# Kernel tuning notes

Measured on AMD Instinct MI355X. Metric: run time of the kernel, lower is better.

## Reference

```python
import jax, jax.numpy as jnp
import numpy as np

H = 32        # num_attention_heads
KVH = 8       # num_key_value_heads
D = 64        # head_dim
HID = 2048    # hidden_size
G = H // KVH  # num_key_value_groups


def setup_inputs() -> dict:
    key = jax.random.key(0)
    k1, k2, k3, k4, k5 = jax.random.split(key, 5)
    B, S = 1, 2048
    s = 1.0 / np.sqrt(HID)
    return {
        "hidden_states": jax.random.normal(k1, (B, S, HID), dtype=jnp.float32),
        "attention_mask": jnp.ones((B, S), dtype=jnp.int32),
        "Wq": jax.random.normal(k2, (H * D, HID), dtype=jnp.float32) * s,
        "Wk": jax.random.normal(k3, (KVH * D, HID), dtype=jnp.float32) * s,
        "Wv": jax.random.normal(k4, (KVH * D, HID), dtype=jnp.float32) * s,
        "Wo": jax.random.normal(k5, (HID, HID), dtype=jnp.float32) * s,
    }


def reference(hidden_states, attention_mask, Wq, Wk, Wv, Wo):
    B, S, _ = hidden_states.shape
    dtype = hidden_states.dtype

    q = (hidden_states @ Wq.T).reshape(B, S, H, D).transpose(0, 2, 1, 3)     # [B,H,S,D]
    k = (hidden_states @ Wk.T).reshape(B, S, KVH, D).transpose(0, 2, 1, 3)   # [B,KVH,S,D]
    v = (hidden_states @ Wv.T).reshape(B, S, KVH, D).transpose(0, 2, 1, 3)

    # repeat_interleave over head dim: each KV head serves G query heads
    k = jnp.repeat(k, G, axis=1)  # [B,H,S,D]
    v = jnp.repeat(v, G, axis=1)

    scores = jnp.einsum('bhqd,bhkd->bhqk', q, k) / np.sqrt(D)  # [B,H,S,S]

    causal = jnp.tril(jnp.ones((S, S), dtype=dtype))                # [S,S]
    am = attention_mask.astype(dtype)[:, None, None, :]              # [B,1,1,S]
    mask = am * causal[None, None, :, :]                             # [B,1,S,S]
    mask = (1.0 - mask) * jnp.finfo(dtype).min
    scores = scores + mask                                           # broadcast over heads

    weights = jax.nn.softmax(scores, axis=-1)
    attn = jnp.einsum('bhqk,bhkd->bhqd', weights, v)                 # [B,H,S,D]
    attn = attn.transpose(0, 2, 1, 3).reshape(B, S, HID)
    return attn @ Wo.T
```

## Files before the change

kernel.cpp:

```cpp
#include <hip/hip_runtime.h>
#include <hip/hip_bf16.h>
#include <math.h>

typedef __attribute__((ext_vector_type(4))) float f32x4;
typedef __attribute__((ext_vector_type(16))) float f32x16;
typedef __attribute__((ext_vector_type(8))) short bf16x8;
typedef __attribute__((ext_vector_type(4))) short s16x4;
typedef __attribute__((ext_vector_type(4))) unsigned int u32x4;
typedef __attribute__((ext_vector_type(2))) unsigned int u32x2;
typedef short s16;
typedef unsigned int u32;
typedef unsigned short u16;

#define S_LEN 2048
#define HIDN  2048
#define QKVW  3072
#define NH    32
#define NKVH  8
#define HD    64

__device__ __forceinline__ s16 f2bf(float f) {
  unsigned int u = __float_as_uint(f);
  unsigned int lsb = (u >> 16) & 1u;
  u += 0x7fffu + lsb;
  return (s16)(u >> 16);
}

__device__ __forceinline__ u32 cvtpk(float lo, float hi) {
  u32 r;
  asm("v_cvt_pk_bf16_f32 %0, %1, %2" : "=v"(r) : "v"(lo), "v"(hi));
  return r;
}

__device__ __forceinline__ void gload16(const void* g, void* l) {
  __builtin_amdgcn_global_load_lds(
      (const __attribute__((address_space(1))) void*)g,
      (__attribute__((address_space(3))) void*)l, 16, 0, 0);
}

__device__ __forceinline__ void pls(u32& a, u32& b) {
  asm volatile("v_permlane32_swap_b32 %0, %1" : "+v"(a), "+v"(b));
}

__device__ __forceinline__ int swz7(int row) { return (row ^ (row >> 3)) & 7; }

__global__ __launch_bounds__(256) void cvt_all(const float* __restrict__ h,
                                               const float* __restrict__ wq,
                                               const float* __restrict__ wk,
                                               const float* __restrict__ wv,
                                               const float* __restrict__ wo,
                                               s16x4* __restrict__ dst) {
  int i = blockIdx.x * 256 + threadIdx.x;
  const float* src; int off;
  if (i < 1048576)      { src = h;  off = i; }
  else if (i < 2097152) { src = wq; off = i - 1048576; }
  else if (i < 2359296) { src = wk; off = i - 2097152; }
  else if (i < 2621440) { src = wv; off = i - 2359296; }
  else                  { src = wo; off = i - 2621440; }
  if (i < 3670016) {
    float4 f = reinterpret_cast<const float4*>(src)[off];
    s16x4 o;
    o.x = f2bf(f.x); o.y = f2bf(f.y); o.z = f2bf(f.z); o.w = f2bf(f.w);
    dst[i] = o;
  }
}

__device__ __forceinline__ void storeC(s16* C, size_t idx, float v)   { C[idx] = f2bf(v); }
__device__ __forceinline__ void storeC(float* C, size_t idx, float v) { C[idx] = v; }

template <typename OUT_T>
__global__ __launch_bounds__(512) void gemm_bt(const s16* __restrict__ A,
                                               const s16* __restrict__ B,
                                               OUT_T* __restrict__ C,
                                               int M, int N, int K, int gridX) {
  __shared__ alignas(16) s16 As[2][8192];
  __shared__ alignas(16) s16 Bs[2][8192];

  const int nwg  = (M >> 7) * gridX;
  const int flat = blockIdx.x;
  const int q8   = nwg >> 3;
  const int swz  = (flat & 7) * q8 + (flat >> 3);
  const int bm   = (swz / gridX) * 128;
  const int bn   = (swz % gridX) * 128;

  const int t    = threadIdx.x;
  const int lane = t & 63;
  const int w    = t >> 6;
  const int wr   = (w >> 2) * 64;
  const int wc   = (w & 3) * 32;
  const int lr   = lane & 15;
  const int lg   = lane >> 4;

  const int srow0 = (w * 2) * 8 + (lane >> 3);
  const int srow1 = (w * 2 + 1) * 8 + (lane >> 3);
  const int sl0   = ((lane & 7) ^ swz7(srow0)) * 8;
  const int sl1   = ((lane & 7) ^ swz7(srow1)) * 8;

  f32x4 acc[4][2];
#pragma unroll
  for (int m = 0; m < 4; ++m)
#pragma unroll
    for (int n = 0; n < 2; ++n)
      acc[m][n] = (f32x4){0.f, 0.f, 0.f, 0.f};

  const int nK = K >> 6;
  int buf = 0;

  {
    gload16(&A[(size_t)(bm + srow0) * K + sl0], (char*)As[0] + (w * 2) * 1024);
    gload16(&A[(size_t)(bm + srow1) * K + sl1], (char*)As[0] + (w * 2 + 1) * 1024);
    gload16(&B[(size_t)(bn + srow0) * K + sl0], (char*)Bs[0] + (w * 2) * 1024);
    gload16(&B[(size_t)(bn + srow1) * K + sl1], (char*)Bs[0] + (w * 2 + 1) * 1024);
  }
  __syncthreads();

  for (int ki = 0; ki < nK; ++ki) {
    if (ki + 1 < nK) {
      const int kt = (ki + 1) << 6;
      gload16(&A[(size_t)(bm + srow0) * K + kt + sl0], (char*)As[buf ^ 1] + (w * 2) * 1024);
      gload16(&A[(size_t)(bm + srow1) * K + kt + sl1], (char*)As[buf ^ 1] + (w * 2 + 1) * 1024);
      gload16(&B[(size_t)(bn + srow0) * K + kt + sl0], (char*)Bs[buf ^ 1] + (w * 2) * 1024);
      gload16(&B[(size_t)(bn + srow1) * K + kt + sl1], (char*)Bs[buf ^ 1] + (w * 2 + 1) * 1024);
    }

    bf16x8 af[4][2], bfr[2][2];
#pragma unroll
    for (int kk = 0; kk < 2; ++kk) {
#pragma unroll
      for (int m = 0; m < 4; ++m) {
        int row = wr + m * 16 + lr;
        af[m][kk] = *(bf16x8*)((char*)As[buf] + row * 128 + (((kk * 4 + lg) ^ swz7(row)) << 4));
      }
#pragma unroll
      for (int n = 0; n < 2; ++n) {
        int row = wc + n * 16 + lr;
        bfr[n][kk] = *(bf16x8*)((char*)Bs[buf] + row * 128 + (((kk * 4 + lg) ^ swz7(row)) << 4));
      }
    }

    __builtin_amdgcn_s_setprio(1);
#pragma unroll
    for (int m = 0; m < 4; ++m)
#pragma unroll
      for (int n = 0; n < 2; ++n)
#pragma unroll
        for (int kk = 0; kk < 2; ++kk)
          acc[m][n] = __builtin_amdgcn_mfma_f32_16x16x32_bf16(af[m][kk], bfr[n][kk], acc[m][n], 0, 0, 0);
    __builtin_amdgcn_s_setprio(0);

    __syncthreads();
    buf ^= 1;
  }

#pragma unroll
  for (int m = 0; m < 4; ++m)
#pragma unroll
    for (int n = 0; n < 2; ++n) {
      int row = bm + wr + m * 16 + lg * 4;
      int col = bn + wc + n * 16 + lr;
#pragma unroll
      for (int j = 0; j < 4; ++j)
        storeC(C, (size_t)(row + j) * N + col, acc[m][n][j]);
    }
}

__global__ __launch_bounds__(512) void attn_kernel(
    const s16* __restrict__ QKV,
    const int* __restrict__ am,
    s16* __restrict__ Ob) {
  __shared__ alignas(16) char smem[65536];
  __shared__ float2 mlb[4][64];

  const int t    = threadIdx.x;
  const int g    = t >> 8;
  const int tg   = t & 255;
  const int lane = t & 63;
  const int w    = tg >> 6;
  const int col  = lane & 31;
  const int hi   = lane >> 5;

  const int hk = blockIdx.x;
  const int p  = blockIdx.y;
  const int h  = hk * 4 + w;
  const int kbase = 2048 + hk * 64;
  const int vbase = 2560 + hk * 64;
  const float CF = 0.18033688f;

  const int krow   = lane >> 3;
  const int kslotb = lane & 7;
  const int vkv    = 2 * (tg >> 3);
  const int vd8    = (tg & 7) * 8;

  for (int phase = 0; phase < 2; ++phase) {
    const int qt = phase ? p : 63 - p;
    const int nt = (qt >> 1) + 1;
    const int R  = (nt + 1) >> 1;
    const int qrow = qt * 32 + col;

    bf16x8 qf[4];
#pragma unroll
    for (int ds = 0; ds < 4; ++ds)
      qf[ds] = *(const bf16x8*)&QKV[(size_t)qrow * QKVW + h * 64 + ds * 16 + hi * 8];

    if (g < nt) {
      char* Kn = smem + (g * 2 + 0) * 16384;
      char* Vn = Kn + 8192;
#pragma unroll
      for (int pp = 0; pp < 2; ++pp) {
        int c   = w * 2 + pp;
        int row = c * 8 + krow;
        int slot = kslotb ^ swz7(row);
        gload16(&QKV[(size_t)(g * 64 + row) * QKVW + kbase + slot * 8], Kn + c * 1024);
      }
      bf16x8 va = *(const bf16x8*)&QKV[(size_t)(g * 64 + vkv) * QKVW + vbase + vd8];
      bf16x8 vb = *(const bf16x8*)&QKV[(size_t)(g * 64 + vkv + 1) * QKVW + vbase + vd8];
#pragma unroll
      for (int i = 0; i < 8; ++i) {
        int d = vd8 + i;
        u32 pk = (u32)(u16)va[i] | ((u32)(u16)vb[i] << 16);
        *(u32*)&Vn[(d * 128 + vkv * 2) ^ (swz7(d) << 4)] = pk;
      }
    }
    int acur = am[g * 64 + lane];

    float m_i = -1e30f, l_part = 0.f;
    f32x16 Oacc[2];
#pragma unroll
    for (int b = 0; b < 2; ++b)
#pragma unroll
      for (int i = 0; i < 16; ++i) Oacc[b][i] = 0.f;
    __syncthreads();

    for (int it = 0; it < R; ++it) {
      const int buf  = it & 1;
      const int tile = 2 * it + g;
      const bool valid = (tile < nt);
      const int kv0  = tile * 64;
      const bool pre = (tile + 2 < nt);

      char* Kc = smem + (g * 2 + buf) * 16384;
      char* Vc = Kc + 8192;
      char* Kn = smem + (g * 2 + (buf ^ 1)) * 16384;
      char* Vn = Kn + 8192;

      bf16x8 va, vb;
      int anext = 0;
      if (pre) {
        const int nk0 = kv0 + 128;
#pragma unroll
        for (int pp = 0; pp < 2; ++pp) {
          int c   = w * 2 + pp;
          int row = c * 8 + krow;
          int slot = kslotb ^ swz7(row);
          gload16(&QKV[(size_t)(nk0 + row) * QKVW + kbase + slot * 8], Kn + c * 1024);
        }
        va = *(const bf16x8*)&QKV[(size_t)(nk0 + vkv) * QKVW + vbase + vd8];
        vb = *(const bf16x8*)&QKV[(size_t)(nk0 + vkv + 1) * QKVW + vbase + vd8];
        anext = am[nk0 + lane];
      }

      if (valid) {
        f32x16 s0, s1;
#pragma unroll
        for (int i = 0; i < 16; ++i) { s0[i] = 0.f; s1[i] = 0.f; }
        __builtin_amdgcn_s_setprio(1);
#pragma unroll
        for (int ds = 0; ds < 4; ++ds) {
          int off = ds * 32 + hi * 16;
          bf16x8 k0 = *(bf16x8*)&Kc[(col * 128 + off) ^ (swz7(col) << 4)];
          bf16x8 k1 = *(bf16x8*)&Kc[((32 + col) * 128 + off) ^ (swz7(32 + col) << 4)];
          s0 = __builtin_amdgcn_mfma_f32_32x32x16_bf16(k0, qf[ds], s0, 0, 0, 0);
          s1 = __builtin_amdgcn_mfma_f32_32x32x16_bf16(k1, qf[ds], s1, 0, 0, 0);
        }
        __builtin_amdgcn_s_setprio(0);

        float pvv[32];
        unsigned long long m64 = __ballot(acur != 0);
        bool interior = (kv0 + 64 <= qt * 32) && (m64 == ~0ull);
        if (interior) {
#pragma unroll
          for (int r = 0; r < 16; ++r) { pvv[r] = s0[r]; pvv[16 + r] = s1[r]; }
        } else {
#pragma unroll
          for (int b = 0; b < 2; ++b)
#pragma unroll
            for (int r = 0; r < 16; ++r) {
              int kvl = b * 32 + (r & 3) + 8 * (r >> 2) + 4 * hi;
              float sv = b ? s1[r] : s0[r];
              bool ok = (kvl + kv0 <= qrow) && ((m64 >> kvl) & 1ull);
              pvv[b * 16 + r] = ok ? sv : -INFINITY;
            }
        }

        float a0 = pvv[0], a1 = pvv[1], a2 = pvv[2], a3 = pvv[3];
#pragma unroll
        for (int i = 4; i < 32; i += 4) {
          a0 = fmaxf(a0, pvv[i]);     a1 = fmaxf(a1, pvv[i + 1]);
          a2 = fmaxf(a2, pvv[i + 2]); a3 = fmaxf(a3, pvv[i + 3]);
        }
        float lmax = fmaxf(fmaxf(a0, a1), fmaxf(a2, a3));
        lmax = fmaxf(lmax, __shfl_xor(lmax, 32));
        float lmaxs = lmax * CF;

        if (!__all(lmaxs - m_i <= 8.f)) {
          float nm = fmaxf(m_i, lmaxs);
          float al = __builtin_amdgcn_exp2f(m_i - nm);
          m_i = nm;
          l_part *= al;
#pragma unroll
          for (int b = 0; b < 2; ++b)
#pragma unroll
            for (int i = 0; i < 16; ++i) Oacc[b][i] *= al;
        }

        float t0 = 0.f, t1 = 0.f, t2 = 0.f, t3 = 0.f;
#pragma unroll
        for (int i = 0; i < 32; i += 4) {
          pvv[i]     = __builtin_amdgcn_exp2f(__builtin_fmaf(pvv[i],     CF, -m_i)); t0 += pvv[i];
          pvv[i + 1] = __builtin_amdgcn_exp2f(__builtin_fmaf(pvv[i + 1], CF, -m_i)); t1 += pvv[i + 1];
          pvv[i + 2] = __builtin_amdgcn_exp2f(__builtin_fmaf(pvv[i + 2], CF, -m_i)); t2 += pvv[i + 2];
          pvv[i + 3] = __builtin_amdgcn_exp2f(__builtin_fmaf(pvv[i + 3], CF, -m_i)); t3 += pvv[i + 3];
        }
        l_part += (t0 + t1) + (t2 + t3);

        bf16x8 pf[4];
#pragma unroll
        for (int b = 0; b < 2; ++b)
#pragma unroll
          for (int gg = 0; gg < 2; ++gg) {
            int base = b * 16 + gg * 8;
            u32 A1 = cvtpk(pvv[base + 0], pvv[base + 1]);
            u32 A2 = cvtpk(pvv[base + 2], pvv[base + 3]);
            u32 B1 = cvtpk(pvv[base + 4], pvv[base + 5]);
            u32 B2 = cvtpk(pvv[base + 6], pvv[base + 7]);
            pls(A1, B1);
            pls(A2, B2);
            u32x4 pw; pw[0] = A1; pw[1] = A2; pw[2] = B1; pw[3] = B2;
            pf[b * 2 + gg] = *reinterpret_cast<bf16x8*>(&pw);
          }

        __builtin_amdgcn_s_setprio(1);
#pragma unroll
        for (int ks = 0; ks < 4; ++ks) {
          int off = ks * 32 + hi * 16;
#pragma unroll
          for (int db = 0; db < 2; ++db) {
            int d = db * 32 + col;
            bf16x8 vf = *(bf16x8*)&Vc[(d * 128 + off) ^ (swz7(d) << 4)];
            Oacc[db] = __builtin_amdgcn_mfma_f32_32x32x16_bf16(vf, pf[ks], Oacc[db], 0, 0, 0);
          }
        }
        __builtin_amdgcn_s_setprio(0);
      }

      if (pre) {
#pragma unroll
        for (int i = 0; i < 8; ++i) {
          int d = vd8 + i;
          u32 pk = (u32)(u16)va[i] | ((u32)(u16)vb[i] << 16);
          *(u32*)&Vn[(d * 128 + vkv * 2) ^ (swz7(d) << 4)] = pk;
        }
        acur = anext;
      }
      __syncthreads();
    }

    float l_p = l_part + __shfl_xor(l_part, 32);

    if (g == 0) {
      float* pool = (float*)smem + w * 2176 + lane * 33;
#pragma unroll
      for (int b = 0; b < 2; ++b)
#pragma unroll
        for (int i = 0; i < 16; ++i) pool[b * 16 + i] = Oacc[b][i];
      mlb[w][lane] = make_float2(m_i, l_p);
    }
    __syncthreads();
    if (g == 1) {
      const float* pool = (const float*)smem + w * 2176 + lane * 33;
      float2 ml0 = mlb[w][lane];
      float mm = fmaxf(ml0.x, m_i);
      float b0 = __builtin_amdgcn_exp2f(ml0.x - mm);
      float b1 = __builtin_amdgcn_exp2f(m_i - mm);
      float linv = 1.0f / (ml0.y * b0 + l_p * b1);
      float sc0 = b0 * linv, sc1 = b1 * linv;
#pragma unroll
      for (int db = 0; db < 2; ++db)
#pragma unroll
        for (int qd = 0; qd < 4; ++qd) {
          float o0 = pool[db * 16 + qd * 4 + 0] * sc0 + Oacc[db][qd * 4 + 0] * sc1;
          float o1 = pool[db * 16 + qd * 4 + 1] * sc0 + Oacc[db][qd * 4 + 1] * sc1;
          float o2 = pool[db * 16 + qd * 4 + 2] * sc0 + Oacc[db][qd * 4 + 2] * sc1;
          float o3 = pool[db * 16 + qd * 4 + 3] * sc0 + Oacc[db][qd * 4 + 3] * sc1;
          u32x2 o;
          o[0] = cvtpk(o0, o1);
          o[1] = cvtpk(o2, o3);
          int d0 = db * 32 + qd * 8 + hi * 4;
          *(u32x2*)&Ob[(size_t)qrow * HIDN + h * 64 + d0] = o;
        }
    }
    __syncthreads();
  }
}

extern "C" void kernel_launch(void* const* d_in, const int* in_sizes, int n_in,
                              void* d_out, int out_size, void* d_ws, size_t ws_size,
                              hipStream_t stream) {
  const float* hidden = (const float*)d_in[0];
  const int*   am     = (const int*)d_in[1];
  const float* Wq     = (const float*)d_in[2];
  const float* Wk     = (const float*)d_in[3];
  const float* Wv     = (const float*)d_in[4];
  const float* Wo     = (const float*)d_in[5];
  float* out = (float*)d_out;

  s16* hb    = (s16*)d_ws;
  s16* wqkvb = hb    + 4194304;
  s16* wob   = wqkvb + 6291456;
  s16* QKVb  = wob   + 4194304;
  s16* Ab    = QKVb  + 6291456;

  cvt_all<<<14336, 256, 0, stream>>>(hidden, Wq, Wk, Wv, Wo, (s16x4*)d_ws);

  gemm_bt<s16><<<384, 512, 0, stream>>>(hb, wqkvb, QKVb, 2048, 3072, 2048, 24);

  attn_kernel<<<dim3(8, 32), 512, 0, stream>>>(QKVb, am, Ab);

  gemm_bt<float><<<256, 512, 0, stream>>>(Ab, wob, out, 2048, 2048, 2048, 16);
}
```

Before: 131.2 us.

## Split attention KV loop across three wave groups instead of two

Raises the attention block from 512 to 768 threads so three groups of four waves each handle every third KV tile, with their own double-buffered K/V shared memory. The final combine now merges three partial softmax states (max, sum, output) through shared memory instead of two. The goal is shorter per-block KV loops and more parallelism per query tile. The cost is more LDS per block (96KB), fewer resident blocks per CU, and a heavier three-way reduction.

```diff
diff --git a/kernel.cpp b/kernel.cpp
--- a/kernel.cpp
+++ b/kernel.cpp
@@ -164,12 +164,12 @@
     }
 }
 
-__global__ __launch_bounds__(512) void attn_kernel(
+__global__ __launch_bounds__(768) void attn_kernel(
     const s16* __restrict__ QKV,
     const int* __restrict__ am,
     s16* __restrict__ Ob) {
-  __shared__ alignas(16) char smem[65536];
-  __shared__ float2 mlb[4][64];
+  __shared__ alignas(16) char smem[98304];
+  __shared__ float2 mlb[2][4][64];
 
   const int t    = threadIdx.x;
   const int g    = t >> 8;
@@ -191,10 +191,12 @@
   const int vkv    = 2 * (tg >> 3);
   const int vd8    = (tg & 7) * 8;
 
+  char* gbase = smem + g * 32768;
+
   for (int phase = 0; phase < 2; ++phase) {
     const int qt = phase ? p : 63 - p;
     const int nt = (qt >> 1) + 1;
-    const int R  = (nt + 1) >> 1;
+    const int R  = (nt + 2) / 3;
     const int qrow = qt * 32 + col;
 
     bf16x8 qf[4];
@@ -203,7 +205,7 @@
       qf[ds] = *(const bf16x8*)&QKV[(size_t)qrow * QKVW + h * 64 + ds * 16 + hi * 8];
 
     if (g < nt) {
-      char* Kn = smem + (g * 2 + 0) * 16384;
+      char* Kn = gbase;
       char* Vn = Kn + 8192;
 #pragma unroll
       for (int pp = 0; pp < 2; ++pp) {
@@ -233,20 +235,20 @@
 
     for (int it = 0; it < R; ++it) {
       const int buf  = it & 1;
-      const int tile = 2 * it + g;
+      const int tile = 3 * it + g;
       const bool valid = (tile < nt);
       const int kv0  = tile * 64;
-      const bool pre = (tile + 2 < nt);
-
-      char* Kc = smem + (g * 2 + buf) * 16384;
+      const bool pre = (tile + 3 < nt);
+
+      char* Kc = gbase + buf * 16384;
       char* Vc = Kc + 8192;
-      char* Kn = smem + (g * 2 + (buf ^ 1)) * 16384;
+      char* Kn = gbase + (buf ^ 1) * 16384;
       char* Vn = Kn + 8192;
 
       bf16x8 va, vb;
       int anext = 0;
       if (pre) {
-        const int nk0 = kv0 + 128;
+        const int nk0 = kv0 + 192;
 #pragma unroll
         for (int pp = 0; pp < 2; ++pp) {
           int c   = w * 2 + pp;
@@ -367,31 +369,34 @@
 
     float l_p = l_part + __shfl_xor(l_part, 32);
 
-    if (g == 0) {
-      float* pool = (float*)smem + w * 2176 + lane * 33;
+    if (g < 2) {
+      float* pool = (float*)(smem + g * 33792) + w * 2112 + lane * 33;
 #pragma unroll
       for (int b = 0; b < 2; ++b)
 #pragma unroll
         for (int i = 0; i < 16; ++i) pool[b * 16 + i] = Oacc[b][i];
-      mlb[w][lane] = make_float2(m_i, l_p);
+      mlb[g][w][lane] = make_float2(m_i, l_p);
     }
     __syncthreads();
-    if (g == 1) {
-      const float* pool = (const float*)smem + w * 2176 + lane * 33;
-      float2 ml0 = mlb[w][lane];
-      float mm = fmaxf(ml0.x, m_i);
+    if (g == 2) {
+      const float* p0 = (float*)(smem + 0)     + w * 2112 + lane * 33;
+      const float* p1 = (float*)(smem + 33792) + w * 2112 + lane * 33;
+      float2 ml0 = mlb[0][w][lane];
+      float2 ml1 = mlb[1][w][lane];
+      float mm = fmaxf(fmaxf(ml0.x, ml1.x), m_i);
       float b0 = __builtin_amdgcn_exp2f(ml0.x - mm);
-      float b1 = __builtin_amdgcn_exp2f(m_i - mm);
-      float linv = 1.0f / (ml0.y * b0 + l_p * b1);
-      float sc0 = b0 * linv, sc1 = b1 * linv;
+      float b1 = __builtin_amdgcn_exp2f(ml1.x - mm);
+      float b2 = __builtin_amdgcn_exp2f(m_i - mm);
+      float linv = 1.0f / (ml0.y * b0 + ml1.y * b1 + l_p * b2);
+      b0 *= linv; b1 *= linv; b2 *= linv;
 #pragma unroll
       for (int db = 0; db < 2; ++db)
 #pragma unroll
         for (int qd = 0; qd < 4; ++qd) {
-          float o0 = pool[db * 16 + qd * 4 + 0] * sc0 + Oacc[db][qd * 4 + 0] * sc1;
-          float o1 = pool[db * 16 + qd * 4 + 1] * sc0 + Oacc[db][qd * 4 + 1] * sc1;
-          float o2 = pool[db * 16 + qd * 4 + 2] * sc0 + Oacc[db][qd * 4 + 2] * sc1;
-          float o3 = pool[db * 16 + qd * 4 + 3] * sc0 + Oacc[db][qd * 4 + 3] * sc1;
+          float o0 = p0[db * 16 + qd * 4 + 0] * b0 + p1[db * 16 + qd * 4 + 0] * b1 + Oacc[db][qd * 4 + 0] * b2;
+          float o1 = p0[db * 16 + qd * 4 + 1] * b0 + p1[db * 16 + qd * 4 + 1] * b1 + Oacc[db][qd * 4 + 1] * b2;
+          float o2 = p0[db * 16 + qd * 4 + 2] * b0 + p1[db * 16 + qd * 4 + 2] * b1 + Oacc[db][qd * 4 + 2] * b2;
+          float o3 = p0[db * 16 + qd * 4 + 3] * b0 + p1[db * 16 + qd * 4 + 3] * b1 + Oacc[db][qd * 4 + 3] * b2;
           u32x2 o;
           o[0] = cvtpk(o0, o1);
           o[1] = cvtpk(o2, o3);
@@ -424,7 +429,7 @@
 
   gemm_bt<s16><<<384, 512, 0, stream>>>(hb, wqkvb, QKVb, 2048, 3072, 2048, 24);
 
-  attn_kernel<<<dim3(8, 32), 512, 0, stream>>>(QKVb, am, Ab);
+  attn_kernel<<<dim3(8, 32), 768, 0, stream>>>(QKVb, am, Ab);
 
   gemm_bt<float><<<256, 512, 0, stream>>>(Ab, wob, out, 2048, 2048, 2048, 16);
 }
```

Result: slower. 159.6 us (+21.6%).
